# Kernel optimization log

Hardware: AMD Instinct MI355X
Metric: run time of the kernel (lower is better)

## Reference

```python
import jax, jax.numpy as jnp
import numpy as np

N_NODES = 100000
N_EDGES = 1600000
IN_CH = 256
OUT_CH = 32
HEADS = 4
NEG_SLOPE = 0.2


def setup_inputs() -> dict:
    key = jax.random.key(0)
    k1, k2, k3, k4, k5 = jax.random.split(key, 5)
    x = jax.random.normal(k1, (N_NODES, IN_CH), dtype=jnp.float32)
    edge_index = jax.random.randint(k2, (2, N_EDGES), 0, N_NODES, dtype=jnp.int64)
    hc = HEADS * OUT_CH
    # glorot init like the torch module
    std_w = np.sqrt(6.0 / (hc + IN_CH))
    W = jax.random.uniform(k3, (hc, IN_CH), dtype=jnp.float32, minval=-std_w, maxval=std_w)
    b = jnp.zeros((hc,), dtype=jnp.float32)
    std_a = np.sqrt(6.0 / (hc + 2))
    att = jax.random.uniform(k4, (hc, 2), dtype=jnp.float32, minval=-std_a, maxval=std_a)
    return {"x": x, "edge_index": edge_index, "W": W, "b": b, "att": att}


def reference(x, edge_index, W, b, att):
    # flow = 'target_to_source': tid=0, sid=1
    tar = edge_index[0]
    src = edge_index[1]
    feat = x @ W.T + b                      # [N, H*C]
    e_pre = feat @ att                      # [N, 2]
    e_src = e_pre[:, 0:1]                   # [N, 1]
    e_tar = e_pre[:, 1:2]                   # [N, 1]
    # edge scores
    e = jnp.exp(jax.nn.leaky_relu(e_src[src] + e_tar[tar], negative_slope=NEG_SLOPE))   # [E, 1]
    e_self = jnp.exp(jax.nn.leaky_relu(e_src + e_tar, negative_slope=NEG_SLOPE))        # [N, 1]
    # softmax denominator over incoming edges + self loop
    e_sum = jax.ops.segment_sum(e, tar, num_segments=N_NODES) + e_self                  # [N, 1]
    alpha_self = e_self / e_sum             # [N, 1]
    alpha = e / e_sum[tar]                  # [E, 1]
    # weighted aggregation (dropout=0 / eval -> identity)
    out = jax.ops.segment_sum(feat[src] * alpha, tar, num_segments=N_NODES)
    out = out + feat * alpha_self           # [N, H*C], concat=True
    return out
```

## Files before the change

kernel.cpp:

```cpp
#include <hip/hip_runtime.h>
#include <hip/hip_bf16.h>
#include <math.h>

#define N_NODES 100000
#define N_EDGES 1600000
#define IN_CH 256
#define HC 128
#define NEG_SLOPE 0.2f

#define NB_C 196
#define CCAP 8704
#define CHUNK 3200

typedef __attribute__((ext_vector_type(8))) short short8;
typedef __attribute__((ext_vector_type(4))) float floatx4;

__device__ inline ushort f2b(float f) {
    __hip_bfloat16 h = __float2bfloat16(f);
    return *(ushort*)&h;
}

__device__ inline float edge_e(float z) {
    float lr = z > 0.f ? z : NEG_SLOPE * z;
    return __expf(lr);
}

__device__ inline float bflo(unsigned u) { return __uint_as_float(u << 16); }
__device__ inline float bfhi(unsigned u) { return __uint_as_float(u & 0xffff0000u); }

__global__ __launch_bounds__(256)
void wconv_k(const float* __restrict__ W, ushort* __restrict__ wb) {
    int i = blockIdx.x * 256 + threadIdx.x;
    float4 v = *(const float4*)&W[(size_t)i * 4];
    ushort4 u;
    u.x = f2b(v.x); u.y = f2b(v.y); u.z = f2b(v.z); u.w = f2b(v.w);
    *(ushort4*)&wb[(size_t)i * 4] = u;
}

#define GBM 128

__global__ __launch_bounds__(256, 2)
void gemm_mfma(const float* __restrict__ x, const ushort* __restrict__ wb,
               const float* __restrict__ b, const float* __restrict__ att,
               __hip_bfloat16* __restrict__ featb,
               float* __restrict__ e_src, float* __restrict__ e_tar,
               float* __restrict__ e_self) {
    __shared__ ushort xs[128][72];
    __shared__ ushort wsh[128][72];

    const int tid  = threadIdx.x;
    const int wave = tid >> 6;
    const int lane = tid & 63;
    const int l16  = lane >> 4;
    const int lc   = lane & 15;
    const int row0 = blockIdx.x * GBM;

    floatx4 acc[2][8];
    #pragma unroll
    for (int mt = 0; mt < 2; ++mt)
        #pragma unroll
        for (int nt = 0; nt < 8; ++nt)
            acc[mt][nt] = (floatx4){0.f, 0.f, 0.f, 0.f};

    for (int kb = 0; kb < 4; ++kb) {
        const int r  = tid >> 4;
        const int kq = tid & 15;
        #pragma unroll
        for (int i = 0; i < 8; ++i) {
            int rr = r + i * 16;
            int gr = row0 + rr;
            float4 v = make_float4(0.f, 0.f, 0.f, 0.f);
            if (gr < N_NODES)
                v = *(const float4*)&x[(size_t)gr * IN_CH + kb * 64 + kq * 4];
            ushort4 u;
            u.x = f2b(v.x); u.y = f2b(v.y); u.z = f2b(v.z); u.w = f2b(v.w);
            *(ushort4*)&xs[rr][kq * 4] = u;
        }
        #pragma unroll
        for (int i = 0; i < 8; ++i) {
            int rr = r + i * 16;
            *(ushort4*)&wsh[rr][kq * 4] =
                *(const ushort4*)&wb[(size_t)rr * IN_CH + kb * 64 + kq * 4];
        }
        __syncthreads();
        #pragma unroll
        for (int ks = 0; ks < 2; ++ks) {
            short8 a0 = *(short8*)&xs[wave * 32 + lc][ks * 32 + l16 * 8];
            short8 a1 = *(short8*)&xs[wave * 32 + 16 + lc][ks * 32 + l16 * 8];
            short8 bf[8];
            #pragma unroll
            for (int nt = 0; nt < 8; ++nt)
                bf[nt] = *(short8*)&wsh[nt * 16 + lc][ks * 32 + l16 * 8];
            #pragma unroll
            for (int nt = 0; nt < 8; ++nt) {
                acc[0][nt] = __builtin_amdgcn_mfma_f32_16x16x32_bf16(a0, bf[nt], acc[0][nt], 0, 0, 0);
                acc[1][nt] = __builtin_amdgcn_mfma_f32_16x16x32_bf16(a1, bf[nt], acc[1][nt], 0, 0, 0);
            }
        }
        __syncthreads();
    }

    float av0[8], av1[8], bc[8];
    #pragma unroll
    for (int nt = 0; nt < 8; ++nt) {
        float2 av = *(const float2*)&att[(nt * 16 + lc) * 2];
        av0[nt] = av.x; av1[nt] = av.y;
        bc[nt] = b[nt * 16 + lc];
    }

    #pragma unroll
    for (int mt = 0; mt < 2; ++mt) {
        #pragma unroll
        for (int rg = 0; rg < 4; ++rg) {
            int row = row0 + wave * 32 + mt * 16 + l16 * 4 + rg;
            float s = 0.f, t = 0.f;
            float vals[8];
            #pragma unroll
            for (int nt = 0; nt < 8; ++nt) {
                float v = acc[mt][nt][rg] + bc[nt];
                vals[nt] = v;
                s += v * av0[nt];
                t += v * av1[nt];
            }
            #pragma unroll
            for (int off = 8; off; off >>= 1) {
                s += __shfl_xor(s, off);
                t += __shfl_xor(t, off);
            }
            if (row < N_NODES) {
                if (lc == 0) {
                    e_src[row] = s;
                    e_tar[row] = t;
                    float z = s + t;
                    float lr = z > 0.f ? z : NEG_SLOPE * z;
                    e_self[row] = __expf(lr);
                }
                #pragma unroll
                for (int nt = 0; nt < 8; ++nt)
                    featb[(size_t)row * HC + nt * 16 + lc] = __float2bfloat16(vals[nt]);
            }
        }
    }
}

__global__ __launch_bounds__(256)
void bin2_k(const int* __restrict__ ei, int* __restrict__ gcur,
            int* __restrict__ ebuf) {
    __shared__ int lcnt[NB_C];
    __shared__ int lcur[NB_C];
    const int base = blockIdx.x * CHUNK;

    for (int i = threadIdx.x; i < NB_C; i += 256) lcnt[i] = 0;
    __syncthreads();

    for (int i = threadIdx.x; i < CHUNK; i += 256)
        atomicAdd(&lcnt[ei[base + i] >> 9], 1);
    __syncthreads();

    for (int bkt = threadIdx.x; bkt < NB_C; bkt += 256) {
        int c = lcnt[bkt];
        lcur[bkt] = c ? atomicAdd(&gcur[bkt], c) : 0;
    }
    __syncthreads();

    for (int i = threadIdx.x; i < CHUNK; i += 256) {
        int t = ei[base + i];
        int s = ei[N_EDGES + base + i];
        int bkt = t >> 9;
        int pos = atomicAdd(&lcur[bkt], 1);
        if (pos < CCAP)
            ebuf[bkt * CCAP + pos] = s | ((t & 511) << 17);
    }
}

__global__ __launch_bounds__(512)
void bucket_csr2_k(const int* __restrict__ gcur, const int* __restrict__ ebuf,
                   const float* __restrict__ e_src, const float* __restrict__ e_tar,
                   int* __restrict__ offsets, int* __restrict__ csr_src,
                   float* __restrict__ ewb) {
    const int b = blockIdx.x;
    const int tid = threadIdx.x;

    __shared__ int sc[256];
    __shared__ int lcnt[512];
    __shared__ int lofs[512];
    __shared__ int lout[CCAP];
    __shared__ float ltar[512];

    {
        int n = b * 512 + tid;
        ltar[tid] = (n < N_NODES) ? e_tar[n] : 0.f;
    }

    if (tid < 256) {
        int c = 0;
        if (tid < NB_C) { c = gcur[tid]; if (c > CCAP) c = CCAP; }
        sc[tid] = c;
    }
    lcnt[tid] = 0;
    __syncthreads();
    #pragma unroll
    for (int off = 1; off < 256; off <<= 1) {
        int v = 0;
        if (tid < 256) v = sc[tid] + ((tid >= off) ? sc[tid - off] : 0);
        __syncthreads();
        if (tid < 256) sc[tid] = v;
        __syncthreads();
    }
    int count = gcur[b]; if (count > CCAP) count = CCAP;
    const int base = (b == 0) ? 0 : sc[b - 1];

    const int* st = &ebuf[b * CCAP];
    for (int i = tid; i < count; i += 512)
        atomicAdd(&lcnt[st[i] >> 17], 1);
    __syncthreads();

    lofs[tid] = lcnt[tid];
    __syncthreads();
    for (int off = 1; off < 512; off <<= 1) {
        int v = lofs[tid] + ((tid >= off) ? lofs[tid - off] : 0);
        __syncthreads();
        lofs[tid] = v;
        __syncthreads();
    }
    int excl = lofs[tid] - lcnt[tid];
    lcnt[tid] = excl;

    {
        int n0 = b * 512 + tid;
        if (n0 < N_NODES) offsets[n0] = base + excl;
    }
    if (b == NB_C - 1 && tid == 0) offsets[N_NODES] = base + count;
    __syncthreads();

    for (int i = tid; i < count; i += 512) {
        int v = st[i];
        int pos = atomicAdd(&lcnt[v >> 17], 1);
        lout[pos] = v;
    }
    __syncthreads();

    for (int i = tid; i < count; i += 512) {
        int v = lout[i];
        int src = v & 0x1FFFF;
        csr_src[base + i] = src;
        ewb[base + i] = edge_e(e_src[src] + ltar[v >> 17]);
    }
}

__global__ __launch_bounds__(256)
void aggregate_k(const int* __restrict__ offsets, const int* __restrict__ csr_src,
                 const float* __restrict__ ewb,
                 const __hip_bfloat16* __restrict__ featb,
                 const float* __restrict__ e_self, float* __restrict__ out) {
    int node = blockIdx.x * 4 + (threadIdx.x >> 6);
    if (node >= N_NODES) return;
    int lane = threadIdx.x & 63;
    int g = lane >> 4;
    int q = lane & 15;
    int beg = offsets[node];
    int end = offsets[node + 1];
    float eself = e_self[node];

    const char* fb = (const char*)featb;
    const size_t qofs = (size_t)(q * 16);

    uint4 su = *(const uint4*)(fb + (size_t)node * 256 + qofs);
    float m0 = (g == 0) ? eself : 0.f;
    float esum = m0;
    float acc[8];
    acc[0] = m0 * bflo(su.x); acc[1] = m0 * bfhi(su.x);
    acc[2] = m0 * bflo(su.y); acc[3] = m0 * bfhi(su.y);
    acc[4] = m0 * bflo(su.z); acc[5] = m0 * bfhi(su.z);
    acc[6] = m0 * bflo(su.w); acc[7] = m0 * bfhi(su.w);

    int j = beg;
    for (; j + 7 < end; j += 8) {
        int s0 = csr_src[j + g];
        int s1 = csr_src[j + 4 + g];
        float e0 = ewb[j + g];
        float e1 = ewb[j + 4 + g];
        uint4 u0 = *(const uint4*)(fb + (size_t)s0 * 256 + qofs);
        uint4 u1 = *(const uint4*)(fb + (size_t)s1 * 256 + qofs);
        esum += e0 + e1;
        acc[0] += e0 * bflo(u0.x) + e1 * bflo(u1.x);
        acc[1] += e0 * bfhi(u0.x) + e1 * bfhi(u1.x);
        acc[2] += e0 * bflo(u0.y) + e1 * bflo(u1.y);
        acc[3] += e0 * bfhi(u0.y) + e1 * bfhi(u1.y);
        acc[4] += e0 * bflo(u0.z) + e1 * bflo(u1.z);
        acc[5] += e0 * bfhi(u0.z) + e1 * bfhi(u1.z);
        acc[6] += e0 * bflo(u0.w) + e1 * bflo(u1.w);
        acc[7] += e0 * bfhi(u0.w) + e1 * bfhi(u1.w);
    }
    for (; j + 3 < end; j += 4) {
        int s0 = csr_src[j + g];
        float e0 = ewb[j + g];
        uint4 u0 = *(const uint4*)(fb + (size_t)s0 * 256 + qofs);
        esum += e0;
        acc[0] += e0 * bflo(u0.x);
        acc[1] += e0 * bfhi(u0.x);
        acc[2] += e0 * bflo(u0.y);
        acc[3] += e0 * bfhi(u0.y);
        acc[4] += e0 * bflo(u0.z);
        acc[5] += e0 * bfhi(u0.z);
        acc[6] += e0 * bflo(u0.w);
        acc[7] += e0 * bfhi(u0.w);
    }
    for (; j < end; ++j) {
        int s0 = csr_src[j];
        float ew = ewb[j];
        uint4 u0 = *(const uint4*)(fb + (size_t)s0 * 256 + qofs);
        float em = (g == 0) ? ew : 0.f;
        esum += em;
        acc[0] += em * bflo(u0.x);
        acc[1] += em * bfhi(u0.x);
        acc[2] += em * bflo(u0.y);
        acc[3] += em * bfhi(u0.y);
        acc[4] += em * bflo(u0.z);
        acc[5] += em * bfhi(u0.z);
        acc[6] += em * bflo(u0.w);
        acc[7] += em * bfhi(u0.w);
    }

    #pragma unroll
    for (int k = 0; k < 8; ++k) {
        acc[k] += __shfl_xor(acc[k], 16);
        acc[k] += __shfl_xor(acc[k], 32);
    }
    esum += __shfl_xor(esum, 16);
    esum += __shfl_xor(esum, 32);

    if (g == 0) {
        float inv = 1.f / esum;
        float* op = &out[(size_t)node * HC + q * 8];
        *(float4*)op = make_float4(acc[0] * inv, acc[1] * inv, acc[2] * inv, acc[3] * inv);
        *(float4*)(op + 4) = make_float4(acc[4] * inv, acc[5] * inv, acc[6] * inv, acc[7] * inv);
    }
}

extern "C" void kernel_launch(void* const* d_in, const int* in_sizes, int n_in,
                              void* d_out, int out_size, void* d_ws, size_t ws_size,
                              hipStream_t stream) {
    const float* x   = (const float*)d_in[0];
    const int*   ei  = (const int*)d_in[1];
    const float* W   = (const float*)d_in[2];
    const float* b   = (const float*)d_in[3];
    const float* att = (const float*)d_in[4];
    float* out = (float*)d_out;

    unsigned char* p = (unsigned char*)d_ws;
    auto take = [&](size_t bytes) {
        unsigned char* r = p;
        p += (bytes + 255) & ~(size_t)255;
        return (void*)r;
    };
    __hip_bfloat16* featb = (__hip_bfloat16*)take((size_t)N_NODES * HC * sizeof(__hip_bfloat16));
    float* e_src   = (float*)take((size_t)N_NODES * sizeof(float));
    float* e_tar   = (float*)take((size_t)N_NODES * sizeof(float));
    float* e_self  = (float*)take((size_t)N_NODES * sizeof(float));
    int*   offsets = (int*)take((size_t)(N_NODES + 1) * sizeof(int));
    int*   gcur    = (int*)take((size_t)NB_C * sizeof(int));
    int*   csr_src = (int*)take((size_t)N_EDGES * sizeof(int));
    float* ewb     = (float*)take((size_t)N_EDGES * sizeof(float));
    int*   ebuf    = (int*)take((size_t)NB_C * CCAP * sizeof(int));
    ushort* wb     = (ushort*)take((size_t)HC * IN_CH * sizeof(ushort));

    (void)hipMemsetAsync(gcur, 0, NB_C * sizeof(int), stream);

    wconv_k<<<(HC * IN_CH) / (256 * 4), 256, 0, stream>>>(W, wb);
    gemm_mfma<<<(N_NODES + GBM - 1) / GBM, 256, 0, stream>>>(x, wb, b, att, featb,
                                                             e_src, e_tar, e_self);

    bin2_k<<<N_EDGES / CHUNK, 256, 0, stream>>>(ei, gcur, ebuf);
    bucket_csr2_k<<<NB_C, 512, 0, stream>>>(gcur, ebuf, e_src, e_tar,
                                            offsets, csr_src, ewb);

    aggregate_k<<<(N_NODES + 3) / 4, 256, 0, stream>>>(offsets, csr_src, ewb,
                                                       featb, e_self, out);
}
```

Baseline: 302.1 us.

## Use finer 128-node buckets for CSR build with separate bucket-offset scan

Raises the bucket count from 196 (512 nodes each) to 782 (128 nodes each), so the CSR-building kernel runs many more, smaller blocks with less shared memory per block. The per-block redundant 256-wide prefix scan over bucket counts moves into a single-block scan kernel that writes bucket base offsets. The aim is more parallelism and occupancy in bucket_csr, at the cost of an extra kernel launch, more global atomics and scattered writes in the binning pass. Per-bucket capacity now has less headroom over the mean bucket size (2432 vs about 2048 expected edges).

```diff
diff --git a/kernel.cpp b/kernel.cpp
--- a/kernel.cpp
+++ b/kernel.cpp
@@ -8,8 +8,8 @@
 #define HC 128
 #define NEG_SLOPE 0.2f
 
-#define NB_C 196
-#define CCAP 8704
+#define NB_F 782
+#define CCAP_F 2432
 #define CHUNK 3200
 
 typedef __attribute__((ext_vector_type(8))) short short8;
@@ -146,18 +146,18 @@
 __global__ __launch_bounds__(256)
 void bin2_k(const int* __restrict__ ei, int* __restrict__ gcur,
             int* __restrict__ ebuf) {
-    __shared__ int lcnt[NB_C];
-    __shared__ int lcur[NB_C];
+    __shared__ int lcnt[NB_F];
+    __shared__ int lcur[NB_F];
     const int base = blockIdx.x * CHUNK;
 
-    for (int i = threadIdx.x; i < NB_C; i += 256) lcnt[i] = 0;
+    for (int i = threadIdx.x; i < NB_F; i += 256) lcnt[i] = 0;
     __syncthreads();
 
     for (int i = threadIdx.x; i < CHUNK; i += 256)
-        atomicAdd(&lcnt[ei[base + i] >> 9], 1);
-    __syncthreads();
-
-    for (int bkt = threadIdx.x; bkt < NB_C; bkt += 256) {
+        atomicAdd(&lcnt[ei[base + i] >> 7], 1);
+    __syncthreads();
+
+    for (int bkt = threadIdx.x; bkt < NB_F; bkt += 256) {
         int c = lcnt[bkt];
         lcur[bkt] = c ? atomicAdd(&gcur[bkt], c) : 0;
     }
@@ -166,81 +166,88 @@
     for (int i = threadIdx.x; i < CHUNK; i += 256) {
         int t = ei[base + i];
         int s = ei[N_EDGES + base + i];
-        int bkt = t >> 9;
+        int bkt = t >> 7;
         int pos = atomicAdd(&lcur[bkt], 1);
-        if (pos < CCAP)
-            ebuf[bkt * CCAP + pos] = s | ((t & 511) << 17);
-    }
-}
-
-__global__ __launch_bounds__(512)
-void bucket_csr2_k(const int* __restrict__ gcur, const int* __restrict__ ebuf,
-                   const float* __restrict__ e_src, const float* __restrict__ e_tar,
-                   int* __restrict__ offsets, int* __restrict__ csr_src,
-                   float* __restrict__ ewb) {
+        if (pos < CCAP_F)
+            ebuf[(size_t)bkt * CCAP_F + pos] = s | ((t & 127) << 17);
+    }
+}
+
+__global__ __launch_bounds__(1024)
+void cscan_k(const int* __restrict__ gcur, int* __restrict__ nbase) {
+    __shared__ int sc[1024];
+    int t = threadIdx.x;
+    int c = 0;
+    if (t < NB_F) { c = gcur[t]; if (c > CCAP_F) c = CCAP_F; }
+    sc[t] = c;
+    __syncthreads();
+    for (int off = 1; off < 1024; off <<= 1) {
+        int v = sc[t] + ((t >= off) ? sc[t - off] : 0);
+        __syncthreads();
+        sc[t] = v;
+        __syncthreads();
+    }
+    if (t < NB_F) {
+        nbase[t] = sc[t] - c;
+        if (t == NB_F - 1) nbase[NB_F] = sc[t];
+    }
+}
+
+__global__ __launch_bounds__(256)
+void bucket_csr_k(const int* __restrict__ gcur, const int* __restrict__ nbase,
+                  const int* __restrict__ ebuf,
+                  const float* __restrict__ e_src, const float* __restrict__ e_tar,
+                  int* __restrict__ offsets, int* __restrict__ csr_src,
+                  float* __restrict__ ewb) {
     const int b = blockIdx.x;
     const int tid = threadIdx.x;
 
-    __shared__ int sc[256];
-    __shared__ int lcnt[512];
-    __shared__ int lofs[512];
-    __shared__ int lout[CCAP];
-    __shared__ float ltar[512];
-
-    {
-        int n = b * 512 + tid;
+    __shared__ int lcnt[128];
+    __shared__ int lofs[128];
+    __shared__ float ltar[128];
+    __shared__ int lout[CCAP_F];
+
+    int count = gcur[b]; if (count > CCAP_F) count = CCAP_F;
+    const int base = nbase[b];
+
+    if (tid < 128) {
+        int n = b * 128 + tid;
         ltar[tid] = (n < N_NODES) ? e_tar[n] : 0.f;
-    }
-
-    if (tid < 256) {
-        int c = 0;
-        if (tid < NB_C) { c = gcur[tid]; if (c > CCAP) c = CCAP; }
-        sc[tid] = c;
-    }
-    lcnt[tid] = 0;
-    __syncthreads();
-    #pragma unroll
-    for (int off = 1; off < 256; off <<= 1) {
+        lcnt[tid] = 0;
+    }
+    __syncthreads();
+
+    const int* st = &ebuf[(size_t)b * CCAP_F];
+    for (int i = tid; i < count; i += 256)
+        atomicAdd(&lcnt[st[i] >> 17], 1);
+    __syncthreads();
+
+    if (tid < 128) lofs[tid] = lcnt[tid];
+    __syncthreads();
+    for (int off = 1; off < 128; off <<= 1) {
         int v = 0;
-        if (tid < 256) v = sc[tid] + ((tid >= off) ? sc[tid - off] : 0);
-        __syncthreads();
-        if (tid < 256) sc[tid] = v;
-        __syncthreads();
-    }
-    int count = gcur[b]; if (count > CCAP) count = CCAP;
-    const int base = (b == 0) ? 0 : sc[b - 1];
-
-    const int* st = &ebuf[b * CCAP];
-    for (int i = tid; i < count; i += 512)
-        atomicAdd(&lcnt[st[i] >> 17], 1);
-    __syncthreads();
-
-    lofs[tid] = lcnt[tid];
-    __syncthreads();
-    for (int off = 1; off < 512; off <<= 1) {
-        int v = lofs[tid] + ((tid >= off) ? lofs[tid - off] : 0);
-        __syncthreads();
-        lofs[tid] = v;
-        __syncthreads();
-    }
-    int excl = lofs[tid] - lcnt[tid];
-    lcnt[tid] = excl;
-
-    {
-        int n0 = b * 512 + tid;
+        if (tid < 128) v = lofs[tid] + ((tid >= off) ? lofs[tid - off] : 0);
+        __syncthreads();
+        if (tid < 128) lofs[tid] = v;
+        __syncthreads();
+    }
+    if (tid < 128) {
+        int excl = lofs[tid] - lcnt[tid];
+        lcnt[tid] = excl;
+        int n0 = b * 128 + tid;
         if (n0 < N_NODES) offsets[n0] = base + excl;
     }
-    if (b == NB_C - 1 && tid == 0) offsets[N_NODES] = base + count;
-    __syncthreads();
-
-    for (int i = tid; i < count; i += 512) {
+    if (b == NB_F - 1 && tid == 0) offsets[N_NODES] = base + count;
+    __syncthreads();
+
+    for (int i = tid; i < count; i += 256) {
         int v = st[i];
         int pos = atomicAdd(&lcnt[v >> 17], 1);
         lout[pos] = v;
     }
     __syncthreads();
 
-    for (int i = tid; i < count; i += 512) {
+    for (int i = tid; i < count; i += 256) {
         int v = lout[i];
         int src = v & 0x1FFFF;
         csr_src[base + i] = src;
@@ -359,21 +366,23 @@
     float* e_tar   = (float*)take((size_t)N_NODES * sizeof(float));
     float* e_self  = (float*)take((size_t)N_NODES * sizeof(float));
     int*   offsets = (int*)take((size_t)(N_NODES + 1) * sizeof(int));
-    int*   gcur    = (int*)take((size_t)NB_C * sizeof(int));
+    int*   gcur    = (int*)take((size_t)NB_F * sizeof(int));
+    int*   nbase   = (int*)take((size_t)(NB_F + 1) * sizeof(int));
     int*   csr_src = (int*)take((size_t)N_EDGES * sizeof(int));
     float* ewb     = (float*)take((size_t)N_EDGES * sizeof(float));
-    int*   ebuf    = (int*)take((size_t)NB_C * CCAP * sizeof(int));
+    int*   ebuf    = (int*)take((size_t)NB_F * CCAP_F * sizeof(int));
     ushort* wb     = (ushort*)take((size_t)HC * IN_CH * sizeof(ushort));
 
-    (void)hipMemsetAsync(gcur, 0, NB_C * sizeof(int), stream);
+    (void)hipMemsetAsync(gcur, 0, NB_F * sizeof(int), stream);
 
     wconv_k<<<(HC * IN_CH) / (256 * 4), 256, 0, stream>>>(W, wb);
     gemm_mfma<<<(N_NODES + GBM - 1) / GBM, 256, 0, stream>>>(x, wb, b, att, featb,
                                                              e_src, e_tar, e_self);
 
     bin2_k<<<N_EDGES / CHUNK, 256, 0, stream>>>(ei, gcur, ebuf);
-    bucket_csr2_k<<<NB_C, 512, 0, stream>>>(gcur, ebuf, e_src, e_tar,
-                                            offsets, csr_src, ewb);
+    cscan_k<<<1, 1024, 0, stream>>>(gcur, nbase);
+    bucket_csr_k<<<NB_F, 256, 0, stream>>>(gcur, nbase, ebuf, e_src, e_tar,
+                                           offsets, csr_src, ewb);
 
     aggregate_k<<<(N_NODES + 3) / 4, 256, 0, stream>>>(offsets, csr_src, ewb,
                                                        featb, e_self, out);
```

Result: slower. 313.3 us (+3.7%).
